# Performance work log

Hardware: AMD Instinct MI355X
Metric: run time of the kernel (lower is better)

Reference implementation:

```python
import jax, jax.numpy as jnp
import numpy as np

NHEAD = 8
DMODEL = 512
DK = DMODEL // NHEAD  # 64

def setup_inputs() -> dict:
    key = jax.random.key(0)
    ks = jax.random.split(key, 7)
    B, S = 4, 2048
    Q = jax.random.normal(ks[0], (B, S, DMODEL), dtype=jnp.float32)
    K = jax.random.normal(ks[1], (B, S, DMODEL), dtype=jnp.float32)
    V = jax.random.normal(ks[2], (B, S, DMODEL), dtype=jnp.float32)
    # Original uses torch.rand (uniform [0,1)) for all weights.
    WQ = jax.random.uniform(ks[3], (NHEAD, DMODEL, DK), dtype=jnp.float32)
    WK = jax.random.uniform(ks[4], (NHEAD, DMODEL, DK), dtype=jnp.float32)
    WV = jax.random.uniform(ks[5], (NHEAD, DMODEL, DK), dtype=jnp.float32)
    WO = jax.random.uniform(ks[6], (NHEAD * DK, DMODEL), dtype=jnp.float32)
    return {"Q": Q, "K": K, "V": V, "WQ": WQ, "WK": WK, "WV": WV, "WO": WO}

def reference(Q, K, V, WQ, WK, WV, WO):
    # Stacked per-head projections: [B,H,S,dk]
    Qh = jnp.einsum('bsd,hdk->bhsk', Q, WQ)
    Kh = jnp.einsum('bsd,hdk->bhsk', K, WK)
    Vh = jnp.einsum('bsd,hdk->bhsk', V, WV)
    dk = Kh.shape[-1]
    scores = jnp.einsum('bhqk,bhsk->bhqs', Qh, Kh) / jnp.sqrt(jnp.float32(dk))
    attn = jax.nn.softmax(scores, axis=-1)  # dropout omitted (eval / deterministic baseline)
    out = jnp.einsum('bhqs,bhsk->bhqk', attn, Vh)
    B, H, S, Dk = out.shape
    out = out.transpose(0, 2, 1, 3).reshape(B, S, H * Dk)  # concat heads on last dim
    return out @ WO
```

## Files before the change

### kernel.cpp

```cpp
#include <hip/hip_runtime.h>

#define NB 4
#define NS 2048
#define ND 512
#define NH 8
#define NDK 64

typedef __attribute__((ext_vector_type(8))) short bf16x8;
typedef __attribute__((ext_vector_type(4))) short bf16x4;
typedef __attribute__((ext_vector_type(4))) float f32x4;
typedef __attribute__((ext_vector_type(4))) int   i32x4;

__device__ inline f32x4 mfma16(bf16x8 a, bf16x8 b, f32x4 c) {
    return __builtin_amdgcn_mfma_f32_16x16x32_bf16(a, b, c, 0, 0, 0);
}
__device__ inline unsigned short f2bf(float f) {
    unsigned u = __float_as_uint(f);
    unsigned r = u + 0x7FFFu + ((u >> 16) & 1u);
    return (unsigned short)(r >> 16);
}
__device__ inline float bf2f(unsigned short h) {
    return __uint_as_float(((unsigned)h) << 16);
}
__device__ inline void splitf(float x, short& hi, short& lo) {
    unsigned short h = f2bf(x);
    hi = (short)h;
    lo = (short)f2bf(x - bf2f(h));
}
__device__ inline float exp2_fast(float x) {
    float r; asm("v_exp_f32 %0, %1" : "=v"(r) : "v"(x)); return r;
}

__global__ __launch_bounds__(256) void prep_w(
    const float* __restrict__ WQ, const float* __restrict__ WK,
    const float* __restrict__ WV,
    short* __restrict__ wqh, short* __restrict__ wql,
    short* __restrict__ wkh, short* __restrict__ wkl, short* __restrict__ wv)
{
    const int z = blockIdx.y;
    const int gid = blockIdx.x * 256 + threadIdx.x;
    const int idx = gid * 4;
    const int dk = idx & 63;
    const int d  = (idx >> 6) & 511;
    const int h  = idx >> 15;
    const float* src = ((z == 0) ? WQ : (z == 1) ? WK : WV) + idx;
    float4 f = *(const float4*)src;
    size_t o = (size_t)(h * 64 + dk) * 512 + d;
    if (z < 2) {
        short* oh = z ? wkh : wqh;
        short* ol = z ? wkl : wql;
        short hh, ll;
        splitf(f.x, hh, ll); oh[o]        = hh; ol[o]        = ll;
        splitf(f.y, hh, ll); oh[o +  512] = hh; ol[o +  512] = ll;
        splitf(f.z, hh, ll); oh[o + 1024] = hh; ol[o + 1024] = ll;
        splitf(f.w, hh, ll); oh[o + 1536] = hh; ol[o + 1536] = ll;
    } else {
        wv[o]        = (short)f2bf(f.x);
        wv[o +  512] = (short)f2bf(f.y);
        wv[o + 1024] = (short)f2bf(f.z);
        wv[o + 1536] = (short)f2bf(f.w);
    }
}

__global__ __launch_bounds__(256, 2) void proj(
    const float* __restrict__ Q, const float* __restrict__ K,
    const float* __restrict__ V,
    const short* __restrict__ wqh, const short* __restrict__ wql,
    const short* __restrict__ wkh, const short* __restrict__ wkl,
    const short* __restrict__ wvp,
    short* __restrict__ qth, short* __restrict__ qtl,
    short* __restrict__ kth, short* __restrict__ ktl, short* __restrict__ vt)
{
    const int z  = blockIdx.z;
    const int m0 = blockIdx.x * 128;
    const int nb = blockIdx.y * 128;
    const int tid = threadIdx.x;
    const int w = tid >> 6, lane = tid & 63, c = lane & 15, g = lane >> 4;
    const int wm = w >> 1, wn = w & 1;

    const float* X  = (z == 0) ? Q : (z == 1) ? K : V;
    const short* Wh = (z == 0) ? wqh : (z == 1) ? wkh : wvp;
    const short* Wl = (z == 0) ? wql : wkl;

    __shared__ __align__(16) short smem[20480];
    short* sxh = smem;
    short* sxl = smem + 5120;
    short* swh = smem + 10240;
    short* swl = smem + 15360;

    f32x4 acc[4][4];
    #pragma unroll
    for (int i = 0; i < 4; i++)
        #pragma unroll
        for (int j = 0; j < 4; j++) acc[i][j] = f32x4{0.f, 0.f, 0.f, 0.f};

    const int r_ = tid >> 1, kq = (tid & 1) * 16;

    bf16x8 axh0, axh1, axl0, axl1;
    bf16x8 awh0, awh1, awl0, awl1;

    auto LD = [&](int k0) {
        const float* s1 = X + (size_t)(m0 + r_) * ND + k0 + kq;
        float4 f0 = ((const float4*)s1)[0];
        float4 f1 = ((const float4*)s1)[1];
        float4 f2 = ((const float4*)s1)[2];
        float4 f3 = ((const float4*)s1)[3];
        float xv[16] = {f0.x,f0.y,f0.z,f0.w, f1.x,f1.y,f1.z,f1.w,
                        f2.x,f2.y,f2.z,f2.w, f3.x,f3.y,f3.z,f3.w};
        short hv[16], lv[16];
        if (z < 2) {
            #pragma unroll
            for (int j = 0; j < 16; j++) splitf(xv[j], hv[j], lv[j]);
        } else {
            #pragma unroll
            for (int j = 0; j < 16; j++) hv[j] = (short)f2bf(xv[j]);
        }
        #pragma unroll
        for (int j = 0; j < 8; j++) {
            axh0[j] = hv[j]; axh1[j] = hv[8 + j];
            if (z < 2) { axl0[j] = lv[j]; axl1[j] = lv[8 + j]; }
        }
        const short* ws1 = Wh + (size_t)(nb + r_) * ND + k0 + kq;
        awh0 = *(const bf16x8*)ws1; awh1 = *(const bf16x8*)(ws1 + 8);
        if (z < 2) {
            const short* ws2 = Wl + (size_t)(nb + r_) * ND + k0 + kq;
            awl0 = *(const bf16x8*)ws2; awl1 = *(const bf16x8*)(ws2 + 8);
        }
    };

    LD(0);

    for (int k0 = 0; k0 < ND; k0 += 32) {
        *(bf16x8*)&sxh[r_*40 + kq]     = axh0;
        *(bf16x8*)&sxh[r_*40 + kq + 8] = axh1;
        *(bf16x8*)&swh[r_*40 + kq]     = awh0;
        *(bf16x8*)&swh[r_*40 + kq + 8] = awh1;
        if (z < 2) {
            *(bf16x8*)&sxl[r_*40 + kq]     = axl0;
            *(bf16x8*)&sxl[r_*40 + kq + 8] = axl1;
            *(bf16x8*)&swl[r_*40 + kq]     = awl0;
            *(bf16x8*)&swl[r_*40 + kq + 8] = awl1;
        }
        __syncthreads();
        if (k0 + 32 < ND) LD(k0 + 32);

        bf16x8 ah[4], al[4];
        #pragma unroll
        for (int mi = 0; mi < 4; mi++) {
            ah[mi] = *(bf16x8*)&sxh[(64*wm + 16*mi + c)*40 + 8*g];
            if (z < 2) al[mi] = *(bf16x8*)&sxl[(64*wm + 16*mi + c)*40 + 8*g];
        }
        #pragma unroll
        for (int nf = 0; nf < 4; nf++) {
            bf16x8 bh = *(bf16x8*)&swh[(64*wn + 16*nf + c)*40 + 8*g];
            if (z < 2) {
                bf16x8 bl = *(bf16x8*)&swl[(64*wn + 16*nf + c)*40 + 8*g];
                #pragma unroll
                for (int mi = 0; mi < 4; mi++) {
                    acc[mi][nf] = mfma16(ah[mi], bh, acc[mi][nf]);
                    acc[mi][nf] = mfma16(ah[mi], bl, acc[mi][nf]);
                    acc[mi][nf] = mfma16(al[mi], bh, acc[mi][nf]);
                }
            } else {
                #pragma unroll
                for (int mi = 0; mi < 4; mi++)
                    acc[mi][nf] = mfma16(ah[mi], bh, acc[mi][nf]);
            }
        }
        __syncthreads();
    }

    const int bbase = (m0 >> 11) * NH;
    const int sbase = m0 & 2047;
    short* ep = smem;
    if (z < 2) {
        #pragma unroll
        for (int pass = 0; pass < 2; pass++) {
            __syncthreads();
            #pragma unroll
            for (int mi = 0; mi < 4; mi++)
                #pragma unroll
                for (int nf = 0; nf < 4; nf++)
                    #pragma unroll
                    for (int r = 0; r < 4; r++) {
                        int rl  = 64*wm + 16*mi + 4*g + r;
                        int col = 64*wn + 16*nf + c;
                        short hh, ll; splitf(acc[mi][nf][r], hh, ll);
                        ep[rl*136 + col] = pass ? ll : hh;
                    }
            __syncthreads();
            int rl2 = tid >> 1, half = tid & 1;
            int head = blockIdx.y * 2 + half;
            int s = sbase + rl2;
            int t = s >> 6, sr = s & 63, sw2 = (sr & 7) << 4;
            short* dst = pass ? (z ? ktl : qtl) : (z ? kth : qth);
            char* base = (char*)dst + ((size_t)(bbase + head) * 32 + t) * 8192 + sr * 128;
            const short* row = &ep[rl2*136 + half*64];
            #pragma unroll
            for (int ch = 0; ch < 8; ch++)
                *(bf16x8*)(base + ((ch*16) ^ sw2)) = *(const bf16x8*)(row + ch*8);
        }
    } else {
        __syncthreads();
        #pragma unroll
        for (int mi = 0; mi < 4; mi++)
            #pragma unroll
            for (int nf = 0; nf < 4; nf++)
                #pragma unroll
                for (int r = 0; r < 4; r++) {
                    int rl  = 64*wm + 16*mi + 4*g + r;
                    int col = 64*wn + 16*nf + c;
                    ep[rl*136 + col] = (short)f2bf(acc[mi][nf][r]);
                }
        __syncthreads();
        int col = tid >> 1, tt = tid & 1;
        int head = blockIdx.y * 2 + (col >> 6), dk = col & 63;
        int s0_ = sbase + tt * 64;
        int t = s0_ >> 6;
        char* base = (char*)vt + ((size_t)(bbase + head) * 32 + t) * 8192 + dk * 128;
        int sw2 = (dk & 7) << 4;
        #pragma unroll
        for (int ch = 0; ch < 8; ch++) {
            bf16x8 vv;
            #pragma unroll
            for (int i = 0; i < 8; i++) vv[i] = ep[(tt*64 + ch*8 + i)*136 + col];
            *(bf16x8*)(base + ((ch*16) ^ sw2)) = vv;
        }
    }
}

__global__ __launch_bounds__(256, 4) void attn_kernel(
    const short* __restrict__ qth, const short* __restrict__ qtl,
    const short* __restrict__ kth, const short* __restrict__ ktl,
    const short* __restrict__ vtl, short* __restrict__ ao)
{
    const int orig = blockIdx.x;
    const int wg = (orig & 7) * 128 + (orig >> 3);
    const int bh = wg >> 5, qb = (wg & 31) * 64;
    const int tid = threadIdx.x;
    const int w = tid >> 6, lane = tid & 63, c = lane & 15, g = lane >> 4;

    __shared__ __align__(16) short kh_s[64*64];
    __shared__ __align__(16) short kl_s[64*64];
    __shared__ __align__(16) short v_s [64*64];
    __shared__ __align__(16) short pb  [4][16*64];
    char* khb = (char*)kh_s;
    char* klb = (char*)kl_s;
    char* vb  = (char*)v_s;
    char* pwb = (char*)pb[w];
    short* pw = pb[w];

    bf16x8 qh[2], ql[2];
    {
        const char* qtbh = (const char*)qth + ((size_t)bh*32 + (qb>>6))*8192;
        const char* qtbl = (const char*)qtl + ((size_t)bh*32 + (qb>>6))*8192;
        int s_in = 16*w + c;
        int sw = (s_in & 7) << 4;
        qh[0] = *(const bf16x8*)(qtbh + s_in*128 + ((16*g) ^ sw));
        qh[1] = *(const bf16x8*)(qtbh + s_in*128 + ((64 + 16*g) ^ sw));
        ql[0] = *(const bf16x8*)(qtbl + s_in*128 + ((16*g) ^ sw));
        ql[1] = *(const bf16x8*)(qtbl + s_in*128 + ((64 + 16*g) ^ sw));
    }

    const char* kg = (const char*)kth + (size_t)bh * 262144;
    const char* lg = (const char*)ktl + (size_t)bh * 262144;
    const char* vg = (const char*)vtl + (size_t)bh * 262144;
    const int thr = w * 2048 + lane * 16;

    const float SC = 0.18033688f;
    float mrow[4], lrowp[4];
    f32x4 acc[4];
    #pragma unroll
    for (int r = 0; r < 4; r++) { mrow[r] = -1e30f; lrowp[r] = 0.f; }
    #pragma unroll
    for (int nf = 0; nf < 4; nf++) acc[nf] = f32x4{0.f,0.f,0.f,0.f};

    i32x4 s0, s1, s2, s3, s4, s5;
    {
        const char* p = kg + thr; s0 = *(const i32x4*)p; s1 = *(const i32x4*)(p + 1024);
        p = lg + thr;             s2 = *(const i32x4*)p; s3 = *(const i32x4*)(p + 1024);
        p = vg + thr;             s4 = *(const i32x4*)p; s5 = *(const i32x4*)(p + 1024);
    }

    for (int t = 0; t < 32; ++t) {
        {
            char* d = khb + thr; *(i32x4*)d = s0; *(i32x4*)(d + 1024) = s1;
            d = klb + thr;       *(i32x4*)d = s2; *(i32x4*)(d + 1024) = s3;
            d = vb + thr;        *(i32x4*)d = s4; *(i32x4*)(d + 1024) = s5;
        }
        __syncthreads();
        if (t < 31) {
            size_t off = (size_t)(t + 1) * 8192 + thr;
            const char* p = kg + off; s0 = *(const i32x4*)p; s1 = *(const i32x4*)(p + 1024);
            p = lg + off;             s2 = *(const i32x4*)p; s3 = *(const i32x4*)(p + 1024);
            p = vg + off;             s4 = *(const i32x4*)p; s5 = *(const i32x4*)(p + 1024);
        }

        f32x4 s4c[4];
        __builtin_amdgcn_s_setprio(1);
        #pragma unroll
        for (int sf = 0; sf < 4; sf++) {
            s4c[sf] = f32x4{0.f,0.f,0.f,0.f};
            int rowK = c + 16*sf;
            #pragma unroll
            for (int ks = 0; ks < 2; ks++) {
                int cb = (ks*64 + 16*g) ^ ((rowK & 7) << 4);
                bf16x8 kh = *(bf16x8*)(khb + rowK*128 + cb);
                bf16x8 kl = *(bf16x8*)(klb + rowK*128 + cb);
                s4c[sf] = mfma16(qh[ks], kh, s4c[sf]);
                s4c[sf] = mfma16(qh[ks], kl, s4c[sf]);
                s4c[sf] = mfma16(ql[ks], kh, s4c[sf]);
            }
        }
        __builtin_amdgcn_s_setprio(0);

        float tmax[4];
        #pragma unroll
        for (int r = 0; r < 4; r++) {
            float v = fmaxf(fmaxf(s4c[0][r], s4c[1][r]), fmaxf(s4c[2][r], s4c[3][r]));
            #pragma unroll
            for (int off = 1; off < 16; off <<= 1) v = fmaxf(v, __shfl_xor(v, off));
            tmax[r] = v;
        }
        float dmax = fmaxf(fmaxf(tmax[0]-mrow[0], tmax[1]-mrow[1]),
                           fmaxf(tmax[2]-mrow[2], tmax[3]-mrow[3]));
        if (!__all(dmax < -144.0f)) {
            if (__any(dmax > 64.0f)) {
                #pragma unroll
                for (int r = 0; r < 4; r++) {
                    float mn = fmaxf(mrow[r], tmax[r]);
                    float fc = exp2_fast((mrow[r] - mn) * SC);
                    mrow[r] = mn; lrowp[r] *= fc;
                    acc[0][r] *= fc; acc[1][r] *= fc; acc[2][r] *= fc; acc[3][r] *= fc;
                }
            }
            float mS[4];
            #pragma unroll
            for (int r = 0; r < 4; r++) mS[r] = mrow[r] * SC;
            float rs[4] = {0.f, 0.f, 0.f, 0.f};
            #pragma unroll
            for (int sf = 0; sf < 4; sf++) {
                #pragma unroll
                for (int r = 0; r < 4; r++) {
                    float p = exp2_fast(fmaf(s4c[sf][r], SC, -mS[r]));
                    rs[r] += p;
                    int q = 4*g + r;
                    *(short*)(pwb + q*128 + ((2*c + 32*sf) ^ ((q & 7) << 4))) =
                        (short)(__float_as_uint(p) >> 16);
                }
            }
            #pragma unroll
            for (int r = 0; r < 4; r++) lrowp[r] += rs[r];

            __builtin_amdgcn_s_setprio(1);
            #pragma unroll
            for (int ks = 0; ks < 2; ks++) {
                int cbp = (ks*64 + 16*g) ^ ((c & 7) << 4);
                bf16x8 pa = *(bf16x8*)(pwb + c*128 + cbp);
                #pragma unroll
                for (int nf = 0; nf < 4; nf++) {
                    int rowV = c + 16*nf;
                    int cbv = (ks*64 + 16*g) ^ ((rowV & 7) << 4);
                    bf16x8 vv = *(bf16x8*)(vb + rowV*128 + cbv);
                    acc[nf] = mfma16(pa, vv, acc[nf]);
                }
            }
            __builtin_amdgcn_s_setprio(0);
        }
        __syncthreads();
    }

    float inv[4];
    #pragma unroll
    for (int r = 0; r < 4; r++) {
        float t2 = lrowp[r];
        #pragma unroll
        for (int off = 1; off < 16; off <<= 1) t2 += __shfl_xor(t2, off);
        inv[r] = 1.f / t2;
    }
    #pragma unroll
    for (int nf = 0; nf < 4; nf++)
        #pragma unroll
        for (int r = 0; r < 4; r++)
            pw[(4*g + r)*64 + c + 16*nf] = (short)f2bf(acc[nf][r] * inv[r]);

    const int b = bh >> 3, hh = bh & 7;
    {
        int q = qb + 16*w + c;
        size_t o = ((size_t)b * NS + q) * ND + hh * NDK + g * 16;
        const short* src = pw + c*64 + g*16;
        *(bf16x8*)&ao[o]     = *(const bf16x8*)src;
        *(bf16x8*)&ao[o + 8] = *(const bf16x8*)(src + 8);
    }
}

__global__ __launch_bounds__(256) void oproj_kernel(
    const short* __restrict__ ao, const float* __restrict__ WO, float* __restrict__ out)
{
    const int orig = blockIdx.x;
    const int wg = (orig & 7) * 64 + (orig >> 3);
    const int mb = (wg >> 3) * 128, nb = (wg & 7) * 64;
    const int tid = threadIdx.x;
    const int w = tid >> 6, lane = tid & 63, c = lane & 15, g = lane >> 4;

    __shared__ __align__(16) short xlds[128*40];
    __shared__ __align__(16) short wt[64*40];

    f32x4 acc[2][4];
    #pragma unroll
    for (int i = 0; i < 2; i++)
        #pragma unroll
        for (int j = 0; j < 4; j++) acc[i][j] = f32x4{0.f,0.f,0.f,0.f};

    for (int k0 = 0; k0 < ND; k0 += 32) {
        {
            int r = tid >> 1, kq = (tid & 1) * 16;
            const short* src = ao + (size_t)(mb + r) * ND + k0 + kq;
            *(bf16x8*)&xlds[r*40 + kq]     = *(const bf16x8*)src;
            *(bf16x8*)&xlds[r*40 + kq + 8] = *(const bf16x8*)(src + 8);
        }
        #pragma unroll
        for (int i = 0; i < 2; i++) {
            int idx = tid * 2 + i;
            int kr = idx >> 4, c4 = (idx & 15) * 4;
            float4 f = *(const float4*)&WO[(size_t)(k0 + kr) * ND + nb + c4];
            wt[(c4+0)*40 + kr] = (short)f2bf(f.x);
            wt[(c4+1)*40 + kr] = (short)f2bf(f.y);
            wt[(c4+2)*40 + kr] = (short)f2bf(f.z);
            wt[(c4+3)*40 + kr] = (short)f2bf(f.w);
        }
        __syncthreads();
        bf16x8 a0 = *(bf16x8*)&xlds[(32*w +      c)*40 + 8*g];
        bf16x8 a1 = *(bf16x8*)&xlds[(32*w + 16 + c)*40 + 8*g];
        #pragma unroll
        for (int nf = 0; nf < 4; nf++) {
            bf16x8 bv = *(bf16x8*)&wt[(c + 16*nf)*40 + 8*g];
            acc[0][nf] = mfma16(a0, bv, acc[0][nf]);
            acc[1][nf] = mfma16(a1, bv, acc[1][nf]);
        }
        __syncthreads();
    }
    #pragma unroll
    for (int mi = 0; mi < 2; mi++)
        #pragma unroll
        for (int nf = 0; nf < 4; nf++)
            #pragma unroll
            for (int r = 0; r < 4; r++) {
                int row = mb + 32*w + 16*mi + 4*g + r;
                out[(size_t)row * ND + nb + c + 16*nf] = acc[mi][nf][r];
            }
}

extern "C" void kernel_launch(void* const* d_in, const int* in_sizes, int n_in,
                              void* d_out, int out_size, void* d_ws, size_t ws_size,
                              hipStream_t stream) {
    (void)in_sizes; (void)n_in; (void)out_size; (void)ws_size;
    const float* Q  = (const float*)d_in[0];
    const float* K  = (const float*)d_in[1];
    const float* V  = (const float*)d_in[2];
    const float* WQ = (const float*)d_in[3];
    const float* WK = (const float*)d_in[4];
    const float* WV = (const float*)d_in[5];
    const float* WO = (const float*)d_in[6];

    char* ws = (char*)d_ws;
    const size_t PLANE = (size_t)NB * NH * NS * NDK * 2;
    short* qth = (short*)(ws);
    short* qtl = (short*)(ws +     PLANE);
    short* kth = (short*)(ws + 2 * PLANE);
    short* ktl = (short*)(ws + 3 * PLANE);
    short* vt  = (short*)(ws + 4 * PLANE);
    short* ao  = (short*)(ws + 5 * PLANE);

    short* wqh = (short*)d_out;
    short* wql = wqh + 262144;
    short* wkh = wqh + 2 * 262144;
    short* wkl = wqh + 3 * 262144;
    short* wv  = wqh + 4 * 262144;

    prep_w<<<dim3(256, 3), 256, 0, stream>>>(WQ, WK, WV, wqh, wql, wkh, wkl, wv);
    proj<<<dim3(64, 4, 3), 256, 0, stream>>>(Q, K, V, wqh, wql, wkh, wkl, wv,
                                             qth, qtl, kth, ktl, vt);
    attn_kernel<<<1024, 256, 0, stream>>>(qth, qtl, kth, ktl, vt, ao);
    oproj_kernel<<<512, 256, 0, stream>>>(ao, WO, (float*)d_out);
}
```

Measured before the change: 274.4 us.

## Pre-split inputs, pipeline proj/oproj with LDS DMA, and defer low-precision score terms

Q and K are now split into bf16 hi/lo planes by a separate prep kernel. The projection kernel loads those planes into double-buffered LDS with global_load_lds, reads weights directly from global, and uses XCD-aware block remapping. The attention kernel computes scores first with hi*hi only and adds the two correction MFMAs only when the tile is not negligible (threshold changed from -144 to -140). The output projection is rewritten with 128x128 tiles and double buffering, and workspace buffers are reassigned into d_out. This trades extra launches and global traffic for fewer conversions and less MFMA work, at the risk of aliasing bugs between buffers and reduced score precision on skipped tiles.

```diff
diff --git a/kernel.cpp b/kernel.cpp
--- a/kernel.cpp
+++ b/kernel.cpp
@@ -29,6 +29,23 @@
 }
 __device__ inline float exp2_fast(float x) {
     float r; asm("v_exp_f32 %0, %1" : "=v"(r) : "v"(x)); return r;
+}
+__device__ inline void gload16(const void* g, void* l) {
+    __builtin_amdgcn_global_load_lds(
+        (const __attribute__((address_space(1))) unsigned int*)g,
+        (__attribute__((address_space(3))) unsigned int*)l, 16, 0, 0);
+}
+
+__global__ __launch_bounds__(256) void prep_split(
+    const float* __restrict__ X, short* __restrict__ xh, short* __restrict__ xl)
+{
+    int i = (blockIdx.x * 256 + threadIdx.x) * 4;
+    float4 f = *(const float4*)(X + i);
+    short h0,h1,h2,h3,l0,l1,l2,l3;
+    splitf(f.x,h0,l0); splitf(f.y,h1,l1); splitf(f.z,h2,l2); splitf(f.w,h3,l3);
+    bf16x4 hv = {h0,h1,h2,h3}, lv = {l0,l1,l2,l3};
+    *(bf16x4*)(xh + i) = hv;
+    *(bf16x4*)(xl + i) = lv;
 }
 
 __global__ __launch_bounds__(256) void prep_w(
@@ -62,99 +79,94 @@
     }
 }
 
-__global__ __launch_bounds__(256, 2) void proj(
-    const float* __restrict__ Q, const float* __restrict__ K,
-    const float* __restrict__ V,
+__global__ __launch_bounds__(256, 3) void proj(
+    const short* __restrict__ xph, const short* __restrict__ xpl,
+    const float* __restrict__ Vf,
     const short* __restrict__ wqh, const short* __restrict__ wql,
     const short* __restrict__ wkh, const short* __restrict__ wkl,
     const short* __restrict__ wvp,
     short* __restrict__ qth, short* __restrict__ qtl,
-    short* __restrict__ kth, short* __restrict__ ktl, short* __restrict__ vt)
+    short* __restrict__ kth, short* __restrict__ ktl,
+    short* __restrict__ vt, int zbase)
 {
-    const int z  = blockIdx.z;
-    const int m0 = blockIdx.x * 128;
-    const int nb = blockIdx.y * 128;
+    const int i = blockIdx.x;
+    const int xcd = i & 7, jj_ = i >> 3;
+    const int nb4 = jj_ & 3, gl = jj_ >> 2;
+    const int grp = gl * 8 + xcd;
+    const int mt = grp & 63;
+    const int z  = zbase + (grp >> 6);
+    const int m0 = mt * 128, nb = nb4 * 128;
     const int tid = threadIdx.x;
-    const int w = tid >> 6, lane = tid & 63, c = lane & 15, g = lane >> 4;
+    const int w = tid >> 6, lane = tid & 63, c = lane & 15, gq = lane >> 4;
     const int wm = w >> 1, wn = w & 1;
 
-    const float* X  = (z == 0) ? Q : (z == 1) ? K : V;
     const short* Wh = (z == 0) ? wqh : (z == 1) ? wkh : wvp;
     const short* Wl = (z == 0) ? wql : wkl;
 
-    __shared__ __align__(16) short smem[20480];
-    short* sxh = smem;
-    short* sxl = smem + 5120;
-    short* swh = smem + 10240;
-    short* swl = smem + 15360;
+    __shared__ __align__(16) short smem[17408];
+    char* smem8 = (char*)smem;
 
     f32x4 acc[4][4];
     #pragma unroll
-    for (int i = 0; i < 4; i++)
-        #pragma unroll
-        for (int j = 0; j < 4; j++) acc[i][j] = f32x4{0.f, 0.f, 0.f, 0.f};
-
-    const int r_ = tid >> 1, kq = (tid & 1) * 16;
-
-    bf16x8 axh0, axh1, axl0, axl1;
-    bf16x8 awh0, awh1, awl0, awl1;
-
-    auto LD = [&](int k0) {
-        const float* s1 = X + (size_t)(m0 + r_) * ND + k0 + kq;
-        float4 f0 = ((const float4*)s1)[0];
-        float4 f1 = ((const float4*)s1)[1];
-        float4 f2 = ((const float4*)s1)[2];
-        float4 f3 = ((const float4*)s1)[3];
-        float xv[16] = {f0.x,f0.y,f0.z,f0.w, f1.x,f1.y,f1.z,f1.w,
-                        f2.x,f2.y,f2.z,f2.w, f3.x,f3.y,f3.z,f3.w};
-        short hv[16], lv[16];
-        if (z < 2) {
-            #pragma unroll
-            for (int j = 0; j < 16; j++) splitf(xv[j], hv[j], lv[j]);
-        } else {
-            #pragma unroll
-            for (int j = 0; j < 16; j++) hv[j] = (short)f2bf(xv[j]);
-        }
-        #pragma unroll
-        for (int j = 0; j < 8; j++) {
-            axh0[j] = hv[j]; axh1[j] = hv[8 + j];
-            if (z < 2) { axl0[j] = lv[j]; axl1[j] = lv[8 + j]; }
-        }
-        const short* ws1 = Wh + (size_t)(nb + r_) * ND + k0 + kq;
-        awh0 = *(const bf16x8*)ws1; awh1 = *(const bf16x8*)(ws1 + 8);
-        if (z < 2) {
-            const short* ws2 = Wl + (size_t)(nb + r_) * ND + k0 + kq;
-            awl0 = *(const bf16x8*)ws2; awl1 = *(const bf16x8*)(ws2 + 8);
-        }
-    };
-
-    LD(0);
-
-    for (int k0 = 0; k0 < ND; k0 += 32) {
-        *(bf16x8*)&sxh[r_*40 + kq]     = axh0;
-        *(bf16x8*)&sxh[r_*40 + kq + 8] = axh1;
-        *(bf16x8*)&swh[r_*40 + kq]     = awh0;
-        *(bf16x8*)&swh[r_*40 + kq + 8] = awh1;
-        if (z < 2) {
-            *(bf16x8*)&sxl[r_*40 + kq]     = axl0;
-            *(bf16x8*)&sxl[r_*40 + kq + 8] = axl1;
-            *(bf16x8*)&swl[r_*40 + kq]     = awl0;
-            *(bf16x8*)&swl[r_*40 + kq + 8] = awl1;
-        }
-        __syncthreads();
-        if (k0 + 32 < ND) LD(k0 + 32);
-
+    for (int a = 0; a < 4; a++)
+        #pragma unroll
+        for (int b = 0; b < 4; b++) acc[a][b] = f32x4{0.f,0.f,0.f,0.f};
+
+    const int rowl = lane >> 2;
+    const int jsw  = (lane & 3) ^ (rowl & 3);
+    const int xorc = (c & 3) << 4;
+
+    auto STAGE_G = [&](int buf, int k0) {
+        size_t rb = (size_t)(m0 + w*32 + rowl) * 1024 + (size_t)k0 * 2 + jsw * 16;
+        char* db = smem8 + buf*16384 + w*2048;
+        gload16((const char*)xph + rb,         db);
+        gload16((const char*)xph + rb + 16384, db + 1024);
+        gload16((const char*)xpl + rb,         db + 8192);
+        gload16((const char*)xpl + rb + 16384, db + 9216);
+    };
+
+    const int r_ = tid >> 1, kqs = (tid & 1) * 16;
+    float4 fv0, fv1, fv2, fv3;
+    auto VLOAD = [&](int k0) {
+        const float* s = Vf + (size_t)(m0 + r_) * ND + k0 + kqs;
+        fv0 = ((const float4*)s)[0]; fv1 = ((const float4*)s)[1];
+        fv2 = ((const float4*)s)[2]; fv3 = ((const float4*)s)[3];
+    };
+    auto VWRITE = [&](int buf) {
+        short t[16];
+        t[0]=(short)f2bf(fv0.x);  t[1]=(short)f2bf(fv0.y);
+        t[2]=(short)f2bf(fv0.z);  t[3]=(short)f2bf(fv0.w);
+        t[4]=(short)f2bf(fv1.x);  t[5]=(short)f2bf(fv1.y);
+        t[6]=(short)f2bf(fv1.z);  t[7]=(short)f2bf(fv1.w);
+        t[8]=(short)f2bf(fv2.x);  t[9]=(short)f2bf(fv2.y);
+        t[10]=(short)f2bf(fv2.z); t[11]=(short)f2bf(fv2.w);
+        t[12]=(short)f2bf(fv3.x); t[13]=(short)f2bf(fv3.y);
+        t[14]=(short)f2bf(fv3.z); t[15]=(short)f2bf(fv3.w);
+        bf16x8 a, b;
+        #pragma unroll
+        for (int q = 0; q < 8; q++) { a[q] = t[q]; b[q] = t[8+q]; }
+        char* bp = smem8 + buf*16384 + r_*64;
+        int x0 = ((tid & 1) * 32) ^ ((r_ & 3) << 4);
+        *(bf16x8*)(bp + x0)        = a;
+        *(bf16x8*)(bp + (x0 ^ 16)) = b;
+    };
+
+    auto COMPUTE = [&](int buf, int k0) {
+        const char* xb = smem8 + buf*16384;
         bf16x8 ah[4], al[4];
         #pragma unroll
         for (int mi = 0; mi < 4; mi++) {
-            ah[mi] = *(bf16x8*)&sxh[(64*wm + 16*mi + c)*40 + 8*g];
-            if (z < 2) al[mi] = *(bf16x8*)&sxl[(64*wm + 16*mi + c)*40 + 8*g];
-        }
+            int off = (64*wm + 16*mi + c)*64 + ((16*gq) ^ xorc);
+            ah[mi] = *(const bf16x8*)(xb + off);
+            if (z < 2) al[mi] = *(const bf16x8*)(xb + 8192 + off);
+        }
+        const short* wr  = Wh + (size_t)(nb + 64*wn + c) * 512 + k0 + 8*gq;
+        const short* wr2 = (z < 2) ? (Wl + (size_t)(nb + 64*wn + c) * 512 + k0 + 8*gq) : wr;
         #pragma unroll
         for (int nf = 0; nf < 4; nf++) {
-            bf16x8 bh = *(bf16x8*)&swh[(64*wn + 16*nf + c)*40 + 8*g];
+            bf16x8 bh = *(const bf16x8*)(wr + nf*16*512);
             if (z < 2) {
-                bf16x8 bl = *(bf16x8*)&swl[(64*wn + 16*nf + c)*40 + 8*g];
+                bf16x8 bl = *(const bf16x8*)(wr2 + nf*16*512);
                 #pragma unroll
                 for (int mi = 0; mi < 4; mi++) {
                     acc[mi][nf] = mfma16(ah[mi], bh, acc[mi][nf]);
@@ -167,7 +179,17 @@
                     acc[mi][nf] = mfma16(ah[mi], bh, acc[mi][nf]);
             }
         }
+    };
+
+    if (z < 2) STAGE_G(0, 0); else { VLOAD(0); VWRITE(0); }
+    int cur = 0;
+    for (int it = 0; it < 16; ++it) {
+        int k0 = it * 32;
         __syncthreads();
+        if (it < 15) { if (z < 2) STAGE_G(cur ^ 1, k0 + 32); else VLOAD(k0 + 32); }
+        COMPUTE(cur, k0);
+        if (z == 2 && it < 15) VWRITE(cur ^ 1);
+        cur ^= 1;
     }
 
     const int bbase = (m0 >> 11) * NH;
@@ -183,14 +205,14 @@
                 for (int nf = 0; nf < 4; nf++)
                     #pragma unroll
                     for (int r = 0; r < 4; r++) {
-                        int rl  = 64*wm + 16*mi + 4*g + r;
+                        int rl  = 64*wm + 16*mi + 4*gq + r;
                         int col = 64*wn + 16*nf + c;
                         short hh, ll; splitf(acc[mi][nf][r], hh, ll);
                         ep[rl*136 + col] = pass ? ll : hh;
                     }
             __syncthreads();
             int rl2 = tid >> 1, half = tid & 1;
-            int head = blockIdx.y * 2 + half;
+            int head = nb4 * 2 + half;
             int s = sbase + rl2;
             int t = s >> 6, sr = s & 63, sw2 = (sr & 7) << 4;
             short* dst = pass ? (z ? ktl : qtl) : (z ? kth : qth);
@@ -208,13 +230,13 @@
             for (int nf = 0; nf < 4; nf++)
                 #pragma unroll
                 for (int r = 0; r < 4; r++) {
-                    int rl  = 64*wm + 16*mi + 4*g + r;
+                    int rl  = 64*wm + 16*mi + 4*gq + r;
                     int col = 64*wn + 16*nf + c;
                     ep[rl*136 + col] = (short)f2bf(acc[mi][nf][r]);
                 }
         __syncthreads();
         int col = tid >> 1, tt = tid & 1;
-        int head = blockIdx.y * 2 + (col >> 6), dk = col & 63;
+        int head = nb4 * 2 + (col >> 6), dk = col & 63;
         int s0_ = sbase + tt * 64;
         int t = s0_ >> 6;
         char* base = (char*)vt + ((size_t)(bbase + head) * 32 + t) * 8192 + dk * 128;
@@ -223,7 +245,7 @@
         for (int ch = 0; ch < 8; ch++) {
             bf16x8 vv;
             #pragma unroll
-            for (int i = 0; i < 8; i++) vv[i] = ep[(tt*64 + ch*8 + i)*136 + col];
+            for (int q = 0; q < 8; q++) vv[q] = ep[(tt*64 + ch*8 + q)*136 + col];
             *(bf16x8*)(base + ((ch*16) ^ sw2)) = vv;
         }
     }
@@ -306,10 +328,7 @@
             for (int ks = 0; ks < 2; ks++) {
                 int cb = (ks*64 + 16*g) ^ ((rowK & 7) << 4);
                 bf16x8 kh = *(bf16x8*)(khb + rowK*128 + cb);
-                bf16x8 kl = *(bf16x8*)(klb + rowK*128 + cb);
                 s4c[sf] = mfma16(qh[ks], kh, s4c[sf]);
-                s4c[sf] = mfma16(qh[ks], kl, s4c[sf]);
-                s4c[sf] = mfma16(ql[ks], kh, s4c[sf]);
             }
         }
         __builtin_amdgcn_s_setprio(0);
@@ -324,7 +343,22 @@
         }
         float dmax = fmaxf(fmaxf(tmax[0]-mrow[0], tmax[1]-mrow[1]),
                            fmaxf(tmax[2]-mrow[2], tmax[3]-mrow[3]));
-        if (!__all(dmax < -144.0f)) {
+        if (!__all(dmax < -140.0f)) {
+            __builtin_amdgcn_s_setprio(1);
+            #pragma unroll
+            for (int sf = 0; sf < 4; sf++) {
+                int rowK = c + 16*sf;
+                #pragma unroll
+                for (int ks = 0; ks < 2; ks++) {
+                    int cb = (ks*64 + 16*g) ^ ((rowK & 7) << 4);
+                    bf16x8 kh = *(bf16x8*)(khb + rowK*128 + cb);
+                    bf16x8 kl = *(bf16x8*)(klb + rowK*128 + cb);
+                    s4c[sf] = mfma16(qh[ks], kl, s4c[sf]);
+                    s4c[sf] = mfma16(ql[ks], kh, s4c[sf]);
+                }
+            }
+            __builtin_amdgcn_s_setprio(0);
+
             if (__any(dmax > 64.0f)) {
                 #pragma unroll
                 for (int r = 0; r < 4; r++) {
@@ -394,60 +428,94 @@
     }
 }
 
-__global__ __launch_bounds__(256) void oproj_kernel(
+__global__ __launch_bounds__(256) void oproj(
     const short* __restrict__ ao, const float* __restrict__ WO, float* __restrict__ out)
 {
-    const int orig = blockIdx.x;
-    const int wg = (orig & 7) * 64 + (orig >> 3);
-    const int mb = (wg >> 3) * 128, nb = (wg & 7) * 64;
+    const int i = blockIdx.x;
+    const int xcd = i & 7, jj_ = i >> 3;
+    const int nb4 = jj_ & 3, gl = jj_ >> 2;
+    const int mt = gl * 8 + xcd;
+    const int m0 = mt * 128, nb = nb4 * 128;
     const int tid = threadIdx.x;
-    const int w = tid >> 6, lane = tid & 63, c = lane & 15, g = lane >> 4;
-
-    __shared__ __align__(16) short xlds[128*40];
-    __shared__ __align__(16) short wt[64*40];
-
-    f32x4 acc[2][4];
-    #pragma unroll
-    for (int i = 0; i < 2; i++)
-        #pragma unroll
-        for (int j = 0; j < 4; j++) acc[i][j] = f32x4{0.f,0.f,0.f,0.f};
-
-    for (int k0 = 0; k0 < ND; k0 += 32) {
-        {
-            int r = tid >> 1, kq = (tid & 1) * 16;
-            const short* src = ao + (size_t)(mb + r) * ND + k0 + kq;
-            *(bf16x8*)&xlds[r*40 + kq]     = *(const bf16x8*)src;
-            *(bf16x8*)&xlds[r*40 + kq + 8] = *(const bf16x8*)(src + 8);
-        }
-        #pragma unroll
-        for (int i = 0; i < 2; i++) {
-            int idx = tid * 2 + i;
-            int kr = idx >> 4, c4 = (idx & 15) * 4;
-            float4 f = *(const float4*)&WO[(size_t)(k0 + kr) * ND + nb + c4];
-            wt[(c4+0)*40 + kr] = (short)f2bf(f.x);
-            wt[(c4+1)*40 + kr] = (short)f2bf(f.y);
-            wt[(c4+2)*40 + kr] = (short)f2bf(f.z);
-            wt[(c4+3)*40 + kr] = (short)f2bf(f.w);
-        }
+    const int w = tid >> 6, lane = tid & 63, c = lane & 15, gq = lane >> 4;
+    const int wm = w >> 1, wn = w & 1;
+
+    __shared__ __align__(16) short smem[18432];
+    char* smem8 = (char*)smem;
+    short* wt0 = smem + 8192;
+
+    f32x4 acc[4][4];
+    #pragma unroll
+    for (int a = 0; a < 4; a++)
+        #pragma unroll
+        for (int b = 0; b < 4; b++) acc[a][b] = f32x4{0.f,0.f,0.f,0.f};
+
+    const int rowl = lane >> 2;
+    const int jsw  = (lane & 3) ^ (rowl & 3);
+    const int xorc = (c & 3) << 4;
+
+    auto STAGE_A = [&](int buf, int k0) {
+        size_t rb = (size_t)(m0 + w*32 + rowl) * 1024 + (size_t)k0 * 2 + jsw * 16;
+        char* db = smem8 + buf*8192 + w*2048;
+        gload16((const char*)ao + rb,         db);
+        gload16((const char*)ao + rb + 16384, db + 1024);
+    };
+
+    const int kg = tid >> 5, ng = tid & 31;
+    float4 wf0, wf1, wf2, wf3;
+    auto WLOAD = [&](int k0) {
+        const float* s = WO + (size_t)(k0 + kg*4) * 512 + nb + ng*4;
+        wf0 = *(const float4*)s;
+        wf1 = *(const float4*)(s + 512);
+        wf2 = *(const float4*)(s + 1024);
+        wf3 = *(const float4*)(s + 1536);
+    };
+    auto WWRITE = [&](int buf) {
+        short* wb = wt0 + buf*5120;
+        bf16x4 c0 = {(short)f2bf(wf0.x),(short)f2bf(wf1.x),(short)f2bf(wf2.x),(short)f2bf(wf3.x)};
+        bf16x4 c1 = {(short)f2bf(wf0.y),(short)f2bf(wf1.y),(short)f2bf(wf2.y),(short)f2bf(wf3.y)};
+        bf16x4 c2 = {(short)f2bf(wf0.z),(short)f2bf(wf1.z),(short)f2bf(wf2.z),(short)f2bf(wf3.z)};
+        bf16x4 c3 = {(short)f2bf(wf0.w),(short)f2bf(wf1.w),(short)f2bf(wf2.w),(short)f2bf(wf3.w)};
+        *(bf16x4*)&wb[(ng*4 + 0)*40 + kg*4] = c0;
+        *(bf16x4*)&wb[(ng*4 + 1)*40 + kg*4] = c1;
+        *(bf16x4*)&wb[(ng*4 + 2)*40 + kg*4] = c2;
+        *(bf16x4*)&wb[(ng*4 + 3)*40 + kg*4] = c3;
+    };
+
+    auto COMPUTE = [&](int buf) {
+        const char* ab = smem8 + buf*8192;
+        const short* wb = wt0 + buf*5120;
+        bf16x8 ah[4];
+        #pragma unroll
+        for (int mi = 0; mi < 4; mi++)
+            ah[mi] = *(const bf16x8*)(ab + (64*wm + 16*mi + c)*64 + ((16*gq) ^ xorc));
+        #pragma unroll
+        for (int nf = 0; nf < 4; nf++) {
+            bf16x8 bh = *(const bf16x8*)&wb[(64*wn + 16*nf + c)*40 + 8*gq];
+            #pragma unroll
+            for (int mi = 0; mi < 4; mi++)
+                acc[mi][nf] = mfma16(ah[mi], bh, acc[mi][nf]);
+        }
+    };
+
+    WLOAD(0); STAGE_A(0, 0); WWRITE(0);
+    int cur = 0;
+    for (int it = 0; it < 16; ++it) {
         __syncthreads();
-        bf16x8 a0 = *(bf16x8*)&xlds[(32*w +      c)*40 + 8*g];
-        bf16x8 a1 = *(bf16x8*)&xlds[(32*w + 16 + c)*40 + 8*g];
-        #pragma unroll
-        for (int nf = 0; nf < 4; nf++) {
-            bf16x8 bv = *(bf16x8*)&wt[(c + 16*nf)*40 + 8*g];
-            acc[0][nf] = mfma16(a0, bv, acc[0][nf]);
-            acc[1][nf] = mfma16(a1, bv, acc[1][nf]);
-        }
-        __syncthreads();
-    }
-    #pragma unroll
-    for (int mi = 0; mi < 2; mi++)
+        if (it < 15) { STAGE_A(cur ^ 1, it*32 + 32); WLOAD(it*32 + 32); }
+        COMPUTE(cur);
+        if (it < 15) WWRITE(cur ^ 1);
+        cur ^= 1;
+    }
+
+    #pragma unroll
+    for (int mi = 0; mi < 4; mi++)
         #pragma unroll
         for (int nf = 0; nf < 4; nf++)
             #pragma unroll
             for (int r = 0; r < 4; r++) {
-                int row = mb + 32*w + 16*mi + 4*g + r;
-                out[(size_t)row * ND + nb + c + 16*nf] = acc[mi][nf][r];
+                int row = m0 + 64*wm + 16*mi + 4*gq + r;
+                out[(size_t)row * ND + nb + 64*wn + 16*nf + c] = acc[mi][nf][r];
             }
 }
 
@@ -469,18 +537,24 @@
     short* qtl = (short*)(ws +     PLANE);
     short* kth = (short*)(ws + 2 * PLANE);
     short* ktl = (short*)(ws + 3 * PLANE);
-    short* vt  = (short*)(ws + 4 * PLANE);
-    short* ao  = (short*)(ws + 5 * PLANE);
+    short* xh  = (short*)(ws + 4 * PLANE);
+    short* xl  = (short*)(ws + 5 * PLANE);
+    short* ao  = xh;
 
     short* wqh = (short*)d_out;
     short* wql = wqh + 262144;
     short* wkh = wqh + 2 * 262144;
     short* wkl = wqh + 3 * 262144;
     short* wv  = wqh + 4 * 262144;
+    short* vt  = (short*)((char*)d_out + 3145728);
 
     prep_w<<<dim3(256, 3), 256, 0, stream>>>(WQ, WK, WV, wqh, wql, wkh, wkl, wv);
-    proj<<<dim3(64, 4, 3), 256, 0, stream>>>(Q, K, V, wqh, wql, wkh, wkl, wv,
-                                             qth, qtl, kth, ktl, vt);
+    prep_split<<<4096, 256, 0, stream>>>(Q, xh, xl);
+    proj<<<256, 256, 0, stream>>>(xh, xl, V, wqh, wql, wkh, wkl, wv,
+                                  qth, qtl, kth, ktl, vt, 0);
+    prep_split<<<4096, 256, 0, stream>>>(K, xh, xl);
+    proj<<<512, 256, 0, stream>>>(xh, xl, V, wqh, wql, wkh, wkl, wv,
+                                  qth, qtl, kth, ktl, vt, 1);
     attn_kernel<<<1024, 256, 0, stream>>>(qth, qtl, kth, ktl, vt, ao);
-    oproj_kernel<<<512, 256, 0, stream>>>(ao, WO, (float*)d_out);
-}
+    oproj<<<256, 256, 0, stream>>>(ao, WO, (float*)d_out);
+}
```

New measurement: 326.2 us. +18.9%, slower.
